# Optimization experiments

Hardware: AMD Instinct MI355X
Metric: run time of the kernel (lower is better)

The kernel has to match this reference:

```python
import jax, jax.numpy as jnp
import numpy as np

EMBED_DIM = 512


def setup_inputs() -> dict:
    key = jax.random.key(0)
    k1, k2, k3 = jax.random.split(key, 3)
    B, T, E = 8, 2048, EMBED_DIM
    x = jax.random.normal(k1, (B, T, E), dtype=jnp.float32)
    # Linear weights stored [in, out] (torch stores [out, in]; math is identical via transpose)
    Wq = jax.random.normal(k2, (E, E), dtype=jnp.float32) * (E ** -0.5)
    bq = jnp.zeros((E,), dtype=jnp.float32)
    Wk = jax.random.normal(k3, (E, E), dtype=jnp.float32) * (E ** -0.5)
    bk = jnp.zeros((E,), dtype=jnp.float32)
    return {"x": x, "Wq": Wq, "bq": bq, "Wk": Wk, "bk": bk}


def reference(x, Wq, bq, Wk, bk) -> jnp.ndarray:
    scaling = jnp.float32(EMBED_DIM ** -0.5)
    q = (x @ Wq + bq) * scaling          # [B, T, E]
    k = x @ Wk + bk                       # [B, T, E]
    scores = jnp.einsum("bqe,bke->bqk", q, k)   # [B, T, T]
    attn = jax.nn.softmax(scores, axis=-1)
    return jnp.einsum("bqk,bke->bqe", attn, x)  # V = x
```

## Files before the change

kernel.cpp:

```cpp
#include <hip/hip_runtime.h>
#include <hip/hip_bf16.h>
#include <stdint.h>

#define B_  8
#define T_  2048
#define E_  512

typedef __attribute__((ext_vector_type(8))) __bf16 bf16x8;
typedef __attribute__((ext_vector_type(8))) unsigned short ushort8;
typedef __attribute__((ext_vector_type(4))) unsigned short ushort4v;
typedef __attribute__((ext_vector_type(4))) float f32x4;

__device__ __forceinline__ float bf2f(unsigned short u) {
  union { unsigned int u; float f; } c; c.u = ((unsigned int)u) << 16; return c.f;
}
__device__ __forceinline__ unsigned short f2bf(float f) {
  union { float f; unsigned int u; } c; c.f = f;
  unsigned int u = c.u;
  unsigned int r = (u + 0x7FFFu + ((u >> 16) & 1u)) >> 16;
  return (unsigned short)r;
}

__device__ __forceinline__ void gload_lds16(const void* g, void* l) {
  __builtin_amdgcn_global_load_lds(
      (const __attribute__((address_space(1))) uint32_t*)g,
      (__attribute__((address_space(3))) uint32_t*)l, 16, 0, 0);
}

__device__ __forceinline__ float sum8(bf16x8 v) {
  float s = 0.f;
#pragma unroll
  for (int j = 0; j < 8; ++j) s += (float)v[j];
  return s;
}

__global__ __launch_bounds__(256)
void trans_conv_kernel(const float* __restrict__ x, unsigned short* __restrict__ xbf,
                       unsigned short* __restrict__ xT) {
  __shared__ unsigned short tile[64][66];
  const int t0 = blockIdx.x * 64, e0 = blockIdx.y * 64, b = blockIdx.z;
  const int tid = threadIdx.x;
  const float* xb = x + ((size_t)b * T_ + t0) * E_ + e0;
  unsigned short* xbf_b = xbf + ((size_t)b * T_ + t0) * E_ + e0;
#pragma unroll
  for (int it = 0; it < 4; ++it) {
    int tr = (tid >> 4) + it * 16;
    int ec = (tid & 15) * 4;
    float4 f = *reinterpret_cast<const float4*>(xb + (size_t)tr * E_ + ec);
    ushort4v o;
    o[0] = f2bf(f.x); o[1] = f2bf(f.y); o[2] = f2bf(f.z); o[3] = f2bf(f.w);
    *reinterpret_cast<ushort4v*>(xbf_b + (size_t)tr * E_ + ec) = o;
    tile[ec + 0][tr] = o[0];
    tile[ec + 1][tr] = o[1];
    tile[ec + 2][tr] = o[2];
    tile[ec + 3][tr] = o[3];
  }
  __syncthreads();
  unsigned short* dst = xT + ((size_t)b * E_ + e0) * T_ + t0;
#pragma unroll
  for (int it = 0; it < 2; ++it) {
    int er = (tid >> 3) + it * 32;
    int tg = (tid & 7) * 8;
    ushort8 r;
#pragma unroll
    for (int j = 0; j < 8; ++j) r[j] = tile[er][tg + j];
    *reinterpret_cast<ushort8*>(dst + (size_t)er * T_ + tg) = r;
  }
}

__global__ __launch_bounds__(256)
void conv_w_kernel(const float* __restrict__ Wq, const float* __restrict__ Wk,
                   const float* __restrict__ bq, const float* __restrict__ bk,
                   unsigned short* __restrict__ WT, float* __restrict__ bqk, float scale) {
  int idx = blockIdx.x * 256 + threadIdx.x;
  int n  = idx >> 9;
  int kk = idx & 511;
  float v = (n < E_) ? Wq[kk * E_ + n] * scale : Wk[kk * E_ + (n - E_)];
  WT[idx] = f2bf(v);
  if (idx < 2 * E_) {
    float bv = (idx < E_) ? bq[idx] * scale : bk[idx - E_];
    bqk[idx] = bv;
  }
}

#define READ_A(pp, ha) do {                                                    \
  const int rbase = (pp) * 32768 + aRow + (ha) * 4096;                         \
  _Pragma("unroll") for (int m = 0; m < 4; ++m) {                              \
    aA[m][0] = *reinterpret_cast<const bf16x8*>(&sm[rbase + m * 1024 + aCol0]);\
    aA[m][1] = *reinterpret_cast<const bf16x8*>(&sm[rbase + m * 1024 + aCol1]);\
  } } while (0)

#define READ_B(pp, hb) do {                                                    \
  const int rbase = (pp) * 32768 + bRow + (hb) * 2048;                         \
  _Pragma("unroll") for (int n = 0; n < 2; ++n) {                              \
    bB[hb][n][0] = *reinterpret_cast<const bf16x8*>(&sm[rbase + n * 1024 + aCol0]);\
    bB[hb][n][1] = *reinterpret_cast<const bf16x8*>(&sm[rbase + n * 1024 + aCol1]);\
  } } while (0)

#define MFMA_Q(ha, hb) do {                                                    \
  _Pragma("unroll") for (int m = 0; m < 4; ++m)                                \
  _Pragma("unroll") for (int n = 0; n < 2; ++n) {                              \
    acc[(ha)*4+m][(hb)*2+n] = __builtin_amdgcn_mfma_f32_16x16x32_bf16(         \
        aA[m][0], bB[hb][n][0], acc[(ha)*4+m][(hb)*2+n], 0, 0, 0);             \
    acc[(ha)*4+m][(hb)*2+n] = __builtin_amdgcn_mfma_f32_16x16x32_bf16(         \
        aA[m][1], bB[hb][n][1], acc[(ha)*4+m][(hb)*2+n], 0, 0, 0);             \
  } } while (0)

#define STAGE_OP(gptr, ld, base, kt) do {                                      \
  _Pragma("unroll") for (int h = 0; h < 2; ++h)                                \
  _Pragma("unroll") for (int rr2 = 0; rr2 < 2; ++rr2)                          \
    gload_lds16(gptr + (long long)(h * 128 + rr2 * 64) * (ld) + (long long)(kt) * 64, \
                &sm[(base) + h * 8192 + rr2 * 4096 + wv * 512]);               \
  } while (0)

template<int OUT_BF16, int DO_EXP>
__global__ __launch_bounds__(512)
void gemm256(const unsigned short* __restrict__ A, int lda, long long strA,
             const unsigned short* __restrict__ B, int ldb, long long strB,
             void* __restrict__ Cv, int ldc, long long strC,
             int K, const float* __restrict__ bias, int NBX, int NBY)
{
  __shared__ unsigned short sm[65536];
  const int tid  = threadIdx.x;
  const int lane = tid & 63;
  const int wv   = tid >> 6;
  const int wr   = wv >> 2;
  const int wc   = wv & 3;
  const int fr   = lane & 15;

  const int nwg = gridDim.x, bid = blockIdx.x;
  const int qq = nwg >> 3, rr = nwg & 7, xc = bid & 7, ii = bid >> 3;
  const int wg = (xc < rr ? xc * (qq + 1) : rr * (qq + 1) + (xc - rr) * qq) + ii;
  const int bx = wg % NBX;
  const int tt = wg / NBX;
  const int by = tt % NBY;
  const int bz = tt / NBY;

  const long long m0 = (long long)by * 256;
  const long long n0 = (long long)bx * 256;
  const unsigned short* Ab = A + (long long)bz * strA + m0 * lda;
  const unsigned short* Bb = B + (long long)bz * strB + n0 * ldb;

  const int srow = tid >> 3;
  const int scol = ((tid & 7) * 8) ^ ((srow & 7) << 3);
  const unsigned short* gA = Ab + (long long)srow * lda + scol;
  const unsigned short* gB = Bb + (long long)srow * ldb + scol;

  const int xorc  = (fr & 7) << 3;
  const int q8    = (lane >> 4) * 8;
  const int aCol0 = (q8) ^ xorc;
  const int aCol1 = (32 + q8) ^ xorc;
  const int aRow  = (wr * 128 + fr) * 64;
  const int bRow  = 16384 + (wc * 64 + fr) * 64;

  f32x4 acc[8][4];
#pragma unroll
  for (int i = 0; i < 8; ++i)
#pragma unroll
    for (int j = 0; j < 4; ++j) acc[i][j] = (f32x4){0.f, 0.f, 0.f, 0.f};

  bf16x8 aA[4][2], bB[2][2][2];
  const int NT = K >> 6;

  STAGE_OP(gA, lda, 0, 0);
  STAGE_OP(gB, ldb, 16384, 0);
  asm volatile("s_waitcnt vmcnt(0)" ::: "memory");
  __builtin_amdgcn_s_barrier();

  int p = 0;
  for (int kt = 0; kt < NT; ++kt) {
    const int pn = p ^ 1;
    const int pnb = pn * 32768;
    READ_A(p, 0);
    READ_B(p, 0);
    if (kt + 1 < NT) STAGE_OP(gA, lda, pnb, kt + 1);
    __builtin_amdgcn_s_barrier();
    __builtin_amdgcn_s_setprio(1); MFMA_Q(0, 0); __builtin_amdgcn_s_setprio(0);
    __builtin_amdgcn_s_barrier();
    READ_B(p, 1);
    if (kt + 1 < NT) STAGE_OP(gB, ldb, pnb + 16384, kt + 1);
    __builtin_amdgcn_s_barrier();
    __builtin_amdgcn_s_setprio(1); MFMA_Q(0, 1); __builtin_amdgcn_s_setprio(0);
    __builtin_amdgcn_s_barrier();
    READ_A(p, 1);
    __builtin_amdgcn_s_barrier();
    __builtin_amdgcn_s_setprio(1); MFMA_Q(1, 0); __builtin_amdgcn_s_setprio(0);
    __builtin_amdgcn_s_barrier();
    __builtin_amdgcn_s_setprio(1); MFMA_Q(1, 1); __builtin_amdgcn_s_setprio(0);
    asm volatile("s_waitcnt vmcnt(0)" ::: "memory");
    __builtin_amdgcn_s_barrier();
    p = pn;
  }

  const int rq = (lane >> 4) * 4;
  if (bias) {
#pragma unroll
    for (int nn = 0; nn < 4; ++nn) {
      const float bv = bias[n0 + wc * 64 + (nn >> 1) * 32 + (nn & 1) * 16 + fr];
#pragma unroll
      for (int mm = 0; mm < 8; ++mm)
#pragma unroll
        for (int j = 0; j < 4; ++j) acc[mm][nn][j] += bv;
    }
  }
  if (DO_EXP) {
#pragma unroll
    for (int mm = 0; mm < 8; ++mm)
#pragma unroll
      for (int nn = 0; nn < 4; ++nn)
#pragma unroll
        for (int j = 0; j < 4; ++j) acc[mm][nn][j] = __expf(acc[mm][nn][j]);
  }
  if (OUT_BF16) {
    unsigned short* C = (unsigned short*)Cv + (long long)bz * strC;
#pragma unroll
    for (int mm = 0; mm < 8; ++mm)
#pragma unroll
      for (int j = 0; j < 4; ++j) {
        const long long row = m0 + wr * 128 + (mm >> 2) * 64 + (mm & 3) * 16 + rq + j;
#pragma unroll
        for (int nn = 0; nn < 4; ++nn) {
          const long long col = n0 + wc * 64 + (nn >> 1) * 32 + (nn & 1) * 16 + fr;
          C[row * ldc + col] = f2bf(acc[mm][nn][j]);
        }
      }
  } else {
    float* C = (float*)Cv + (long long)bz * strC;
#pragma unroll
    for (int mm = 0; mm < 8; ++mm)
#pragma unroll
      for (int j = 0; j < 4; ++j) {
        const long long row = m0 + wr * 128 + (mm >> 2) * 64 + (mm & 3) * 16 + rq + j;
#pragma unroll
        for (int nn = 0; nn < 4; ++nn) {
          const long long col = n0 + wc * 64 + (nn >> 1) * 32 + (nn & 1) * 16 + fr;
          C[row * ldc + col] = acc[mm][nn][j];
        }
      }
  }
}

__global__ __launch_bounds__(512)
void gemm_pv(const unsigned short* __restrict__ A, int lda, long long strA,
             const unsigned short* __restrict__ B, int ldb, long long strB,
             float* __restrict__ C, int ldc, long long strC, int K)
{
  __shared__ unsigned short sm[49152];
  const int tid  = threadIdx.x;
  const int lane = tid & 63;
  const int wv   = tid >> 6;
  const int wr   = wv >> 1;
  const int wc   = wv & 1;
  const int fr   = lane & 15;

  const int nwg = gridDim.x, bid = blockIdx.x;
  const int qq = nwg >> 3, rr = nwg & 7, xc = bid & 7, ii = bid >> 3;
  const int wg = (xc < rr ? xc * (qq + 1) : rr * (qq + 1) + (xc - rr) * qq) + ii;
  const int bx = wg & 3;
  const int by = (wg >> 2) & 7;
  const int bz = wg >> 5;

  const long long m0 = (long long)by * 256;
  const long long n0 = (long long)bx * 128;
  const unsigned short* Ab = A + (long long)bz * strA + m0 * lda;
  const unsigned short* Bb = B + (long long)bz * strB + n0 * ldb;

  const int srow = tid >> 3;
  const int scol = ((tid & 7) * 8) ^ ((srow & 7) << 3);
  const unsigned short* gA = Ab + (long long)srow * lda + scol;
  const unsigned short* gB = Bb + (long long)srow * ldb + scol;

  const int xorc  = (fr & 7) << 3;
  const int q8    = (lane >> 4) * 8;
  const int aCol0 = q8 ^ xorc;
  const int aCol1 = (32 + q8) ^ xorc;
  const int aRow  = (wr * 64 + fr) * 64;
  const int bRow  = 16384 + (wc * 64 + fr) * 64;

  f32x4 acc[4][4];
#pragma unroll
  for (int i = 0; i < 4; ++i)
#pragma unroll
    for (int j = 0; j < 4; ++j) acc[i][j] = (f32x4){0.f, 0.f, 0.f, 0.f};
  float rs0 = 0.f, rs1 = 0.f;
  bf16x8 aA[4][2], bB2[2][2];
  const int NT = K >> 6;

#pragma unroll
  for (int r = 0; r < 4; ++r)
    gload_lds16(gA + (long long)(r * 64) * lda, &sm[r * 4096 + wv * 512]);
#pragma unroll
  for (int r = 0; r < 2; ++r)
    gload_lds16(gB + (long long)(r * 64) * ldb, &sm[16384 + r * 4096 + wv * 512]);
  asm volatile("s_waitcnt vmcnt(0)" ::: "memory");
  __builtin_amdgcn_s_barrier();

  int p = 0;
  for (int kt = 0; kt < NT; ++kt) {
    const int pb = p * 24576, pnb = (p ^ 1) * 24576;
    const long long koff = (long long)(kt + 1) * 64;
#pragma unroll
    for (int m = 0; m < 4; ++m) {
      aA[m][0] = *reinterpret_cast<const bf16x8*>(&sm[pb + aRow + m * 1024 + aCol0]);
      aA[m][1] = *reinterpret_cast<const bf16x8*>(&sm[pb + aRow + m * 1024 + aCol1]);
    }
#pragma unroll
    for (int n = 0; n < 2; ++n) {
      bB2[n][0] = *reinterpret_cast<const bf16x8*>(&sm[pb + bRow + n * 1024 + aCol0]);
      bB2[n][1] = *reinterpret_cast<const bf16x8*>(&sm[pb + bRow + n * 1024 + aCol1]);
    }
    if (kt + 1 < NT) {
      gload_lds16(gA + koff,                            &sm[pnb + 0     + wv * 512]);
      gload_lds16(gA + (long long)64  * lda + koff,     &sm[pnb + 4096  + wv * 512]);
      gload_lds16(gB + koff,                            &sm[pnb + 16384 + wv * 512]);
    }
    __builtin_amdgcn_s_barrier();
    __builtin_amdgcn_s_setprio(1);
#pragma unroll
    for (int m = 0; m < 4; ++m)
#pragma unroll
      for (int n = 0; n < 2; ++n) {
        acc[m][n] = __builtin_amdgcn_mfma_f32_16x16x32_bf16(aA[m][0], bB2[n][0], acc[m][n], 0, 0, 0);
        acc[m][n] = __builtin_amdgcn_mfma_f32_16x16x32_bf16(aA[m][1], bB2[n][1], acc[m][n], 0, 0, 0);
      }
    __builtin_amdgcn_s_setprio(0);
    if (wc == 0) { rs0 += sum8(aA[0][0]) + sum8(aA[0][1]); rs1 += sum8(aA[2][0]) + sum8(aA[2][1]); }
    else         { rs0 += sum8(aA[1][0]) + sum8(aA[1][1]); rs1 += sum8(aA[3][0]) + sum8(aA[3][1]); }
    __builtin_amdgcn_s_barrier();
#pragma unroll
    for (int n = 0; n < 2; ++n) {
      bB2[n][0] = *reinterpret_cast<const bf16x8*>(&sm[pb + bRow + (2 + n) * 1024 + aCol0]);
      bB2[n][1] = *reinterpret_cast<const bf16x8*>(&sm[pb + bRow + (2 + n) * 1024 + aCol1]);
    }
    if (kt + 1 < NT) {
      gload_lds16(gA + (long long)128 * lda + koff,     &sm[pnb + 8192        + wv * 512]);
      gload_lds16(gA + (long long)192 * lda + koff,     &sm[pnb + 12288       + wv * 512]);
      gload_lds16(gB + (long long)64  * ldb + koff,     &sm[pnb + 16384 + 4096 + wv * 512]);
    }
    __builtin_amdgcn_s_barrier();
    __builtin_amdgcn_s_setprio(1);
#pragma unroll
    for (int m = 0; m < 4; ++m)
#pragma unroll
      for (int n = 0; n < 2; ++n) {
        acc[m][2 + n] = __builtin_amdgcn_mfma_f32_16x16x32_bf16(aA[m][0], bB2[n][0], acc[m][2 + n], 0, 0, 0);
        acc[m][2 + n] = __builtin_amdgcn_mfma_f32_16x16x32_bf16(aA[m][1], bB2[n][1], acc[m][2 + n], 0, 0, 0);
      }
    __builtin_amdgcn_s_setprio(0);
    asm volatile("s_waitcnt vmcnt(0)" ::: "memory");
    __builtin_amdgcn_s_barrier();
    p ^= 1;
  }

  rs0 += __shfl_xor(rs0, 16); rs0 += __shfl_xor(rs0, 32);
  rs1 += __shfl_xor(rs1, 16); rs1 += __shfl_xor(rs1, 32);
  float* rsl = (float*)sm;
  if (lane < 16) {
    rsl[wr * 64 + wc * 16 + lane]      = rs0;
    rsl[wr * 64 + 32 + wc * 16 + lane] = rs1;
  }
  __syncthreads();

  const int rq = (lane >> 4) * 4;
  float* Cb = C + (long long)bz * strC;
#pragma unroll
  for (int m = 0; m < 4; ++m)
#pragma unroll
    for (int j = 0; j < 4; ++j) {
      const int lrow = wr * 64 + m * 16 + rq + j;
      const float inv = 1.0f / rsl[lrow];
      const long long row = m0 + lrow;
#pragma unroll
      for (int n = 0; n < 4; ++n)
        Cb[row * ldc + n0 + wc * 64 + n * 16 + fr] = acc[m][n][j] * inv;
    }
}

extern "C" void kernel_launch(void* const* d_in, const int* in_sizes, int n_in,
                              void* d_out, int out_size, void* d_ws, size_t ws_size,
                              hipStream_t stream)
{
  const float* x  = (const float*)d_in[0];
  const float* Wq = (const float*)d_in[1];
  const float* bq = (const float*)d_in[2];
  const float* Wk = (const float*)d_in[3];
  const float* bk = (const float*)d_in[4];
  float* out = (float*)d_out;

  char* w = (char*)d_ws;
  unsigned short* xbf  = (unsigned short*)w;  w += (size_t)B_ * T_ * E_ * 2;
  unsigned short* xT   = (unsigned short*)w;  w += (size_t)B_ * T_ * E_ * 2;
  unsigned short* WT   = (unsigned short*)w;  w += (size_t)2 * E_ * E_ * 2;
  float*          bqk  = (float*)w;           w += (size_t)2 * E_ * 4;
  unsigned short* qk   = (unsigned short*)w;  w += (size_t)B_ * T_ * 2 * E_ * 2;
  unsigned short* attn = (unsigned short*)w;  w += (size_t)B_ * T_ * T_ * 2;

  const float scale = 0.044194173824159216f;

  trans_conv_kernel<<<dim3(32, 8, 8), 256, 0, stream>>>(x, xbf, xT);
  conv_w_kernel<<<2048, 256, 0, stream>>>(Wq, Wk, bq, bk, WT, bqk, scale);

  gemm256<1, 0><<<256, 512, 0, stream>>>(
      xbf, E_, 0, WT, E_, 0, qk, 2 * E_, 0, E_, bqk, 4, 64);

  gemm256<1, 1><<<512, 512, 0, stream>>>(
      qk, 2 * E_, (long long)T_ * 2 * E_,
      qk + E_, 2 * E_, (long long)T_ * 2 * E_,
      attn, T_, (long long)T_ * T_, E_, nullptr, 8, 8);

  gemm_pv<<<256, 512, 0, stream>>>(
      attn, T_, (long long)T_ * T_,
      xT, T_, (long long)E_ * T_,
      out, E_, (long long)T_ * E_, T_);
}
```

Before: 140.7 us.

## Compute softmax row sums in the QK epilogue and retile the PV GEMM

```diff
diff --git a/kernel.cpp b/kernel.cpp
--- a/kernel.cpp
+++ b/kernel.cpp
@@ -25,13 +25,6 @@
   __builtin_amdgcn_global_load_lds(
       (const __attribute__((address_space(1))) uint32_t*)g,
       (__attribute__((address_space(3))) uint32_t*)l, 16, 0, 0);
-}
-
-__device__ __forceinline__ float sum8(bf16x8 v) {
-  float s = 0.f;
-#pragma unroll
-  for (int j = 0; j < 8; ++j) s += (float)v[j];
-  return s;
 }
 
 __global__ __launch_bounds__(256)
@@ -118,7 +111,8 @@
 void gemm256(const unsigned short* __restrict__ A, int lda, long long strA,
              const unsigned short* __restrict__ B, int ldb, long long strB,
              void* __restrict__ Cv, int ldc, long long strC,
-             int K, const float* __restrict__ bias, int NBX, int NBY)
+             int K, const float* __restrict__ bias, int NBX, int NBY,
+             float* __restrict__ Rg)
 {
   __shared__ unsigned short sm[65536];
   const int tid  = threadIdx.x;
@@ -238,29 +232,59 @@
         }
       }
   }
-}
-
-__global__ __launch_bounds__(512)
-void gemm_pv(const unsigned short* __restrict__ A, int lda, long long strA,
-             const unsigned short* __restrict__ B, int ldb, long long strB,
-             float* __restrict__ C, int ldc, long long strC, int K)
+  if (DO_EXP) {
+    float* rps = (float*)sm;
+    __syncthreads();
+#pragma unroll
+    for (int mm = 0; mm < 8; ++mm)
+#pragma unroll
+      for (int j = 0; j < 4; ++j) {
+        float s = acc[mm][0][j] + acc[mm][1][j] + acc[mm][2][j] + acc[mm][3][j];
+        s += __shfl_xor(s, 1); s += __shfl_xor(s, 2);
+        s += __shfl_xor(s, 4); s += __shfl_xor(s, 8);
+        const int lrow = wr * 128 + (mm >> 2) * 64 + (mm & 3) * 16 + rq + j;
+        if (fr == 0) rps[wc * 256 + lrow] = s;
+      }
+    __syncthreads();
+    if (tid < 256) {
+      const float s = rps[tid] + rps[256 + tid] + rps[512 + tid] + rps[768 + tid];
+      Rg[((long long)bz * NBX + bx) * 2048 + m0 + tid] = s;
+    }
+  }
+}
+
+__global__ __launch_bounds__(256)
+void rowsum_inv_kernel(const float* __restrict__ R, float* __restrict__ invR) {
+  const int i = blockIdx.x * 256 + threadIdx.x;
+  const int b = i >> 11, t = i & 2047;
+  float s = 0.f;
+#pragma unroll
+  for (int c = 0; c < 8; ++c) s += R[((long long)(b * 8 + c)) * 2048 + t];
+  invR[i] = 1.0f / s;
+}
+
+__global__ __launch_bounds__(256)
+void gemm_pv2(const unsigned short* __restrict__ A, int lda, long long strA,
+              const unsigned short* __restrict__ B, int ldb, long long strB,
+              const float* __restrict__ invR,
+              float* __restrict__ C, int ldc, long long strC, int K)
 {
-  __shared__ unsigned short sm[49152];
+  __shared__ unsigned short sm[32768];
   const int tid  = threadIdx.x;
   const int lane = tid & 63;
   const int wv   = tid >> 6;
-  const int wr   = wv >> 1;
-  const int wc   = wv & 1;
+  const int wrp  = wv >> 1;
+  const int wcp  = wv & 1;
   const int fr   = lane & 15;
 
   const int nwg = gridDim.x, bid = blockIdx.x;
   const int qq = nwg >> 3, rr = nwg & 7, xc = bid & 7, ii = bid >> 3;
   const int wg = (xc < rr ? xc * (qq + 1) : rr * (qq + 1) + (xc - rr) * qq) + ii;
   const int bx = wg & 3;
-  const int by = (wg >> 2) & 7;
-  const int bz = wg >> 5;
-
-  const long long m0 = (long long)by * 256;
+  const int by = (wg >> 2) & 15;
+  const int bz = wg >> 6;
+
+  const long long m0 = (long long)by * 128;
   const long long n0 = (long long)bx * 128;
   const unsigned short* Ab = A + (long long)bz * strA + m0 * lda;
   const unsigned short* Bb = B + (long long)bz * strB + n0 * ldb;
@@ -272,47 +296,47 @@
 
   const int xorc  = (fr & 7) << 3;
   const int q8    = (lane >> 4) * 8;
-  const int aCol0 = q8 ^ xorc;
-  const int aCol1 = (32 + q8) ^ xorc;
-  const int aRow  = (wr * 64 + fr) * 64;
-  const int bRow  = 16384 + (wc * 64 + fr) * 64;
+  const int c0    = q8 ^ xorc;
+  const int c1    = (32 + q8) ^ xorc;
+  const int aRow  = (wrp * 64 + fr) * 64;
+  const int bRow  = 8192 + (wcp * 64 + fr) * 64;
 
   f32x4 acc[4][4];
 #pragma unroll
   for (int i = 0; i < 4; ++i)
 #pragma unroll
     for (int j = 0; j < 4; ++j) acc[i][j] = (f32x4){0.f, 0.f, 0.f, 0.f};
-  float rs0 = 0.f, rs1 = 0.f;
+
   bf16x8 aA[4][2], bB2[2][2];
   const int NT = K >> 6;
 
 #pragma unroll
   for (int r = 0; r < 4; ++r)
-    gload_lds16(gA + (long long)(r * 64) * lda, &sm[r * 4096 + wv * 512]);
-#pragma unroll
-  for (int r = 0; r < 2; ++r)
-    gload_lds16(gB + (long long)(r * 64) * ldb, &sm[16384 + r * 4096 + wv * 512]);
+    gload_lds16(gA + (long long)(r * 32) * lda, &sm[r * 2048 + tid * 8]);
+#pragma unroll
+  for (int r = 0; r < 4; ++r)
+    gload_lds16(gB + (long long)(r * 32) * ldb, &sm[8192 + r * 2048 + tid * 8]);
   asm volatile("s_waitcnt vmcnt(0)" ::: "memory");
   __builtin_amdgcn_s_barrier();
 
   int p = 0;
   for (int kt = 0; kt < NT; ++kt) {
-    const int pb = p * 24576, pnb = (p ^ 1) * 24576;
+    const int pb = p * 16384, pnb = pb ^ 16384;
     const long long koff = (long long)(kt + 1) * 64;
 #pragma unroll
     for (int m = 0; m < 4; ++m) {
-      aA[m][0] = *reinterpret_cast<const bf16x8*>(&sm[pb + aRow + m * 1024 + aCol0]);
-      aA[m][1] = *reinterpret_cast<const bf16x8*>(&sm[pb + aRow + m * 1024 + aCol1]);
+      aA[m][0] = *reinterpret_cast<const bf16x8*>(&sm[pb + aRow + m * 1024 + c0]);
+      aA[m][1] = *reinterpret_cast<const bf16x8*>(&sm[pb + aRow + m * 1024 + c1]);
     }
 #pragma unroll
     for (int n = 0; n < 2; ++n) {
-      bB2[n][0] = *reinterpret_cast<const bf16x8*>(&sm[pb + bRow + n * 1024 + aCol0]);
-      bB2[n][1] = *reinterpret_cast<const bf16x8*>(&sm[pb + bRow + n * 1024 + aCol1]);
+      bB2[n][0] = *reinterpret_cast<const bf16x8*>(&sm[pb + bRow + n * 1024 + c0]);
+      bB2[n][1] = *reinterpret_cast<const bf16x8*>(&sm[pb + bRow + n * 1024 + c1]);
     }
     if (kt + 1 < NT) {
-      gload_lds16(gA + koff,                            &sm[pnb + 0     + wv * 512]);
-      gload_lds16(gA + (long long)64  * lda + koff,     &sm[pnb + 4096  + wv * 512]);
-      gload_lds16(gB + koff,                            &sm[pnb + 16384 + wv * 512]);
+#pragma unroll
+      for (int r = 0; r < 4; ++r)
+        gload_lds16(gA + (long long)(r * 32) * lda + koff, &sm[pnb + r * 2048 + tid * 8]);
     }
     __builtin_amdgcn_s_barrier();
     __builtin_amdgcn_s_setprio(1);
@@ -324,18 +348,16 @@
         acc[m][n] = __builtin_amdgcn_mfma_f32_16x16x32_bf16(aA[m][1], bB2[n][1], acc[m][n], 0, 0, 0);
       }
     __builtin_amdgcn_s_setprio(0);
-    if (wc == 0) { rs0 += sum8(aA[0][0]) + sum8(aA[0][1]); rs1 += sum8(aA[2][0]) + sum8(aA[2][1]); }
-    else         { rs0 += sum8(aA[1][0]) + sum8(aA[1][1]); rs1 += sum8(aA[3][0]) + sum8(aA[3][1]); }
     __builtin_amdgcn_s_barrier();
 #pragma unroll
     for (int n = 0; n < 2; ++n) {
-      bB2[n][0] = *reinterpret_cast<const bf16x8*>(&sm[pb + bRow + (2 + n) * 1024 + aCol0]);
-      bB2[n][1] = *reinterpret_cast<const bf16x8*>(&sm[pb + bRow + (2 + n) * 1024 + aCol1]);
+      bB2[n][0] = *reinterpret_cast<const bf16x8*>(&sm[pb + bRow + (2 + n) * 1024 + c0]);
+      bB2[n][1] = *reinterpret_cast<const bf16x8*>(&sm[pb + bRow + (2 + n) * 1024 + c1]);
     }
     if (kt + 1 < NT) {
-      gload_lds16(gA + (long long)128 * lda + koff,     &sm[pnb + 8192        + wv * 512]);
-      gload_lds16(gA + (long long)192 * lda + koff,     &sm[pnb + 12288       + wv * 512]);
-      gload_lds16(gB + (long long)64  * ldb + koff,     &sm[pnb + 16384 + 4096 + wv * 512]);
+#pragma unroll
+      for (int r = 0; r < 4; ++r)
+        gload_lds16(gB + (long long)(r * 32) * ldb + koff, &sm[pnb + 8192 + r * 2048 + tid * 8]);
     }
     __builtin_amdgcn_s_barrier();
     __builtin_amdgcn_s_setprio(1);
@@ -352,27 +374,18 @@
     p ^= 1;
   }
 
-  rs0 += __shfl_xor(rs0, 16); rs0 += __shfl_xor(rs0, 32);
-  rs1 += __shfl_xor(rs1, 16); rs1 += __shfl_xor(rs1, 32);
-  float* rsl = (float*)sm;
-  if (lane < 16) {
-    rsl[wr * 64 + wc * 16 + lane]      = rs0;
-    rsl[wr * 64 + 32 + wc * 16 + lane] = rs1;
-  }
-  __syncthreads();
-
   const int rq = (lane >> 4) * 4;
   float* Cb = C + (long long)bz * strC;
 #pragma unroll
   for (int m = 0; m < 4; ++m)
 #pragma unroll
     for (int j = 0; j < 4; ++j) {
-      const int lrow = wr * 64 + m * 16 + rq + j;
-      const float inv = 1.0f / rsl[lrow];
+      const int lrow = wrp * 64 + m * 16 + rq + j;
       const long long row = m0 + lrow;
+      const float inv = invR[bz * 2048 + row];
 #pragma unroll
       for (int n = 0; n < 4; ++n)
-        Cb[row * ldc + n0 + wc * 64 + n * 16 + fr] = acc[m][n][j] * inv;
+        Cb[row * ldc + n0 + wcp * 64 + n * 16 + fr] = acc[m][n][j] * inv;
     }
 }
 
@@ -392,6 +405,8 @@
   unsigned short* xT   = (unsigned short*)w;  w += (size_t)B_ * T_ * E_ * 2;
   unsigned short* WT   = (unsigned short*)w;  w += (size_t)2 * E_ * E_ * 2;
   float*          bqk  = (float*)w;           w += (size_t)2 * E_ * 4;
+  float*          R    = (float*)w;           w += (size_t)B_ * 8 * T_ * 4;
+  float*          invR = (float*)w;           w += (size_t)B_ * T_ * 4;
   unsigned short* qk   = (unsigned short*)w;  w += (size_t)B_ * T_ * 2 * E_ * 2;
   unsigned short* attn = (unsigned short*)w;  w += (size_t)B_ * T_ * T_ * 2;
 
@@ -401,15 +416,17 @@
   conv_w_kernel<<<2048, 256, 0, stream>>>(Wq, Wk, bq, bk, WT, bqk, scale);
 
   gemm256<1, 0><<<256, 512, 0, stream>>>(
-      xbf, E_, 0, WT, E_, 0, qk, 2 * E_, 0, E_, bqk, 4, 64);
+      xbf, E_, 0, WT, E_, 0, qk, 2 * E_, 0, E_, bqk, 4, 64, nullptr);
 
   gemm256<1, 1><<<512, 512, 0, stream>>>(
       qk, 2 * E_, (long long)T_ * 2 * E_,
       qk + E_, 2 * E_, (long long)T_ * 2 * E_,
-      attn, T_, (long long)T_ * T_, E_, nullptr, 8, 8);
-
-  gemm_pv<<<256, 512, 0, stream>>>(
+      attn, T_, (long long)T_ * T_, E_, nullptr, 8, 8, R);
+
+  rowsum_inv_kernel<<<64, 256, 0, stream>>>(R, invR);
+
+  gemm_pv2<<<512, 256, 0, stream>>>(
       attn, T_, (long long)T_ * T_,
       xT, T_, (long long)E_ * T_,
-      out, E_, (long long)T_ * E_, T_);
-}
+      invR, out, E_, (long long)T_ * E_, T_);
+}
```

Result: no change. 139.5 us (-0.8%).
